# Kernel tuning notes

Measured on AMD Instinct MI355X. Metric: run time of the kernel, lower is better.

The kernel has to match this reference:

```python
import jax, jax.numpy as jnp
import numpy as np


def setup_inputs() -> dict:
    key = jax.random.key(0)
    ks = jax.random.split(key, 8)
    B, S, Nc, C, Cseed = 4, 4096, 8192, 512, 256
    return {
        "query_xyz": jax.random.normal(ks[0], (B, S, 3), dtype=jnp.float32),
        "ref_xyz": jax.random.normal(ks[1], (B, Nc, 3), dtype=jnp.float32),
        "ref_feat": jax.random.normal(ks[2], (B, C, Nc), dtype=jnp.float32),
        "seed_features": jax.random.normal(ks[3], (B, Cseed, S), dtype=jnp.float32),
        "W_seed_proj": jax.random.normal(ks[4], (Cseed, C), dtype=jnp.float32) * 0.02,
        "b_seed_proj": jax.random.normal(ks[5], (Cseed,), dtype=jnp.float32) * 0.02,
        "W_concat_proj": jax.random.normal(ks[6], (Cseed, 2 * Cseed), dtype=jnp.float32) * 0.02,
        "b_concat_proj": jax.random.normal(ks[7], (Cseed,), dtype=jnp.float32) * 0.02,
    }


def _nn_gather(query_xyz, ref_xyz, ref_feat):
    # torch.cdist(p=2) + argmin: argmin over squared distance is identical
    # (sqrt is monotonic), so we skip the sqrt.
    q2 = jnp.sum(query_xyz * query_xyz, axis=-1, keepdims=True)      # (B,S,1)
    r2 = jnp.sum(ref_xyz * ref_xyz, axis=-1)[:, None, :]             # (B,1,Nc)
    qr = jnp.einsum("bsd,bnd->bsn", query_xyz, ref_xyz)              # (B,S,Nc)
    d2 = q2 + r2 - 2.0 * qr                                          # (B,S,Nc)
    idx = jnp.argmin(d2, axis=-1)                                    # (B,S) int
    # gather nearest-neighbor features: (B,C,Nc) -> (B,C,S)
    return jnp.take_along_axis(ref_feat, idx[:, None, :], axis=2)


def reference(query_xyz, ref_xyz, ref_feat, seed_features,
              W_seed_proj, b_seed_proj, W_concat_proj, b_concat_proj):
    lift3d_raw = _nn_gather(query_xyz, ref_xyz, ref_feat)            # (B,C,S)
    # 1x1 Conv1d == channel matmul
    lift3d_seed = jnp.einsum("oc,bcs->bos", W_seed_proj, lift3d_raw) \
                  + b_seed_proj[None, :, None]                       # (B,256,S)
    fused = jnp.concatenate([seed_features, lift3d_seed], axis=1)    # (B,512,S)
    out = jnp.einsum("oc,bcs->bos", W_concat_proj, fused) \
          + b_concat_proj[None, :, None]                             # (B,256,S)
    return out
```

## Files before the change

### kernel.cpp

```cpp
#include <hip/hip_runtime.h>

#define B_   4
#define S_   4096
#define NC   8192
#define C_   512
#define CS   256
#define KTOT 768

typedef __attribute__((ext_vector_type(8))) short short8;
typedef __attribute__((ext_vector_type(4))) float f32x4;

static __device__ __forceinline__ unsigned short f2bf(float x) {
    unsigned u = __builtin_bit_cast(unsigned, x);
    unsigned r = u + 0x7FFFu + ((u >> 16) & 1u);
    return (unsigned short)(r >> 16);
}

__global__ __launch_bounds__(256) void prep_kernel(
        const float* __restrict__ rxyz, float4* __restrict__ refpk,
        const float* __restrict__ Wcat, const float* __restrict__ Wseed,
        unsigned short* __restrict__ Wcomb,
        const float* __restrict__ bseed, const float* __restrict__ bcat,
        float* __restrict__ beff) {
    __shared__ float sa[64][68];
    __shared__ float sbt[64][68];
    int bid = blockIdx.x;
    int tid = threadIdx.x;

    if (bid < 64) {
        int w = tid >> 6, l = tid & 63;
        int o = bid * 4 + w;
        float4 wv = *(const float4*)(Wcat + (size_t)o * 512 + 256 + l * 4);
        float4 bb = *(const float4*)(bseed + l * 4);
        float acc = __fmul_rn(wv.x, bb.x);
        acc = fmaf(wv.y, bb.y, acc);
        acc = fmaf(wv.z, bb.z, acc);
        acc = fmaf(wv.w, bb.w, acc);
        #pragma unroll
        for (int off = 32; off > 0; off >>= 1) acc += __shfl_down(acc, off);
        if (l == 0) beff[o] = acc + bcat[o];
    } else if (bid < 96) {
        int xb = bid - 64;
        int tc = (xb & 7) * 64;
        int to = (xb >> 3) * 64;
        int tx = tid & 15, ty = tid >> 4;
        float acc[4][4] = {};
        for (int kt = 0; kt < 256; kt += 64) {
            __syncthreads();
            #pragma unroll
            for (int r = 0; r < 4; ++r) {
                int oo = r * 16 + ty;
                float4 v = *(const float4*)(Wcat + (size_t)(to + oo) * 512 + 256 + kt + tx * 4);
                sa[oo][tx * 4 + 0] = v.x;
                sa[oo][tx * 4 + 1] = v.y;
                sa[oo][tx * 4 + 2] = v.z;
                sa[oo][tx * 4 + 3] = v.w;
                float4 u = *(const float4*)(Wseed + (size_t)(kt + oo) * 512 + tc + tx * 4);
                sbt[oo][tx * 4 + 0] = u.x;
                sbt[oo][tx * 4 + 1] = u.y;
                sbt[oo][tx * 4 + 2] = u.z;
                sbt[oo][tx * 4 + 3] = u.w;
            }
            __syncthreads();
            for (int k = 0; k < 64; ++k) {
                float a[4], bb2[4];
                #pragma unroll
                for (int i = 0; i < 4; ++i) a[i] = sa[ty * 4 + i][k];
                #pragma unroll
                for (int j = 0; j < 4; ++j) bb2[j] = sbt[k][tx * 4 + j];
                #pragma unroll
                for (int i = 0; i < 4; ++i)
                    #pragma unroll
                    for (int j = 0; j < 4; ++j)
                        acc[i][j] = fmaf(a[i], bb2[j], acc[i][j]);
            }
        }
        #pragma unroll
        for (int i = 0; i < 4; ++i)
            #pragma unroll
            for (int j = 0; j < 4; ++j)
                Wcomb[(size_t)(to + ty * 4 + i) * KTOT + 256 + tc + tx * 4 + j] = f2bf(acc[i][j]);
    } else if (bid < 160) {
        int g = ((bid - 96) * 256 + tid) * 4;
        int o = g >> 8, cc = g & 255;
        float4 v = *(const float4*)(Wcat + (size_t)o * 512 + cc);
        ushort4 ov;
        ov.x = f2bf(v.x); ov.y = f2bf(v.y); ov.z = f2bf(v.z); ov.w = f2bf(v.w);
        *(ushort4*)(Wcomb + (size_t)o * KTOT + cc) = ov;
    } else {
        int gid = (bid - 160) * 256 + tid;
        float x = rxyz[gid * 3 + 0];
        float y = rxyz[gid * 3 + 1];
        float z = rxyz[gid * 3 + 2];
        float r2 = __fadd_rn(__fadd_rn(__fmul_rn(x, x), __fmul_rn(y, y)), __fmul_rn(z, z));
        refpk[gid] = make_float4(x, y, z, r2);
    }
}

__global__ __launch_bounds__(256) void mid_kernel(
        const float* __restrict__ qxyz, const float4* __restrict__ refpk,
        float* __restrict__ pval, int* __restrict__ pidx,
        const float* __restrict__ rf, unsigned short* __restrict__ refT) {
    __shared__ float t[64][65];
    int bid = blockIdx.x;
    int tid = threadIdx.x;

    if (bid % 3 != 0) {
        int id = bid - bid / 3 - 1;
        int b = id >> 10;
        int c0 = ((id >> 7) & 7) * 64;
        int n0 = (id & 127) * 64;
        int tx = tid & 15, ty = tid >> 4;
        #pragma unroll
        for (int r = 0; r < 4; ++r) {
            int cc = r * 16 + ty;
            float4 v = *(const float4*)(rf + ((size_t)b * C_ + c0 + cc) * NC + n0 + tx * 4);
            t[tx * 4 + 0][cc] = v.x;
            t[tx * 4 + 1][cc] = v.y;
            t[tx * 4 + 2][cc] = v.z;
            t[tx * 4 + 3][cc] = v.w;
        }
        __syncthreads();
        #pragma unroll
        for (int r = 0; r < 4; ++r) {
            int n = r * 16 + ty;
            ushort4 o;
            o.x = f2bf(t[n][tx * 4 + 0]);
            o.y = f2bf(t[n][tx * 4 + 1]);
            o.z = f2bf(t[n][tx * 4 + 2]);
            o.w = f2bf(t[n][tx * 4 + 3]);
            *(ushort4*)(refT + ((size_t)b * NC + n0 + n) * C_ + c0 + tx * 4) = o;
        }
    } else {
        int aid = bid / 3;
        int sblk = aid & 127;
        int c = (aid >> 7) & 3;
        int b = aid >> 9;
        int lane = tid & 63;
        int qg = tid >> 6;
        int sbase = sblk * 32 + qg * 8;

        float qx[8], qy[8], qz[8], q2[8];
        #pragma unroll
        for (int q = 0; q < 8; ++q) {
            const float* qp = qxyz + ((size_t)(b * S_ + sbase + q)) * 3;
            qx[q] = qp[0]; qy[q] = qp[1]; qz[q] = qp[2];
            q2[q] = __fadd_rn(__fadd_rn(__fmul_rn(qx[q], qx[q]), __fmul_rn(qy[q], qy[q])),
                              __fmul_rn(qz[q], qz[q]));
        }

        const float4* ep = refpk + (size_t)b * NC + c * 2048 + lane;
        float best[8];
        int bj[8];
        #pragma unroll
        for (int q = 0; q < 8; ++q) { best[q] = 3.4028235e38f; bj[q] = 0; }

        #pragma unroll 4
        for (int j = 0; j < 32; ++j) {
            float4 r = ep[j * 64];
            #pragma unroll
            for (int q = 0; q < 8; ++q) {
                float qr = __fadd_rn(__fadd_rn(__fmul_rn(qx[q], r.x), __fmul_rn(qy[q], r.y)),
                                     __fmul_rn(qz[q], r.z));
                float s = __fadd_rn(q2[q], r.w);
                float d2 = fmaf(qr, -2.0f, s);
                if (d2 < best[q]) { best[q] = d2; bj[q] = j; }
            }
        }

        int bx[8];
        #pragma unroll
        for (int q = 0; q < 8; ++q) bx[q] = c * 2048 + bj[q] * 64 + lane;

        #pragma unroll
        for (int m = 1; m < 64; m <<= 1) {
            #pragma unroll
            for (int q = 0; q < 8; ++q) {
                float vv = __shfl_xor(best[q], m, 64);
                int xx = __shfl_xor(bx[q], m, 64);
                if (vv < best[q] || (vv == best[q] && xx < bx[q])) {
                    best[q] = vv; bx[q] = xx;
                }
            }
        }
        if (lane == 0) {
            #pragma unroll
            for (int q = 0; q < 8; ++q) {
                int qs = b * S_ + sbase + q;
                pval[qs * 4 + c] = best[q];
                pidx[qs * 4 + c] = bx[q];
            }
        }
    }
}

__global__ __launch_bounds__(256) void fused_gemm_kernel(
        const unsigned short* __restrict__ Wcomb,
        const float* __restrict__ seed,
        const unsigned short* __restrict__ refT,
        const float* __restrict__ pval,
        const int* __restrict__ pidx,
        const float* __restrict__ beff,
        float* __restrict__ out) {
    __shared__ __align__(16) unsigned short sA[128][72];
    __shared__ __align__(16) unsigned short sB[32][72];
    __shared__ int sIdx[32];
    __shared__ float sBias[128];

    int tid = threadIdx.x;
    int b = blockIdx.z;
    int m0 = blockIdx.y * 128;
    int s0 = blockIdx.x * 32;
    if (tid < 32) {
        int qs = b * S_ + s0 + tid;
        float v = pval[qs * 4 + 0];
        int x = pidx[qs * 4 + 0];
        #pragma unroll
        for (int c = 1; c < 4; ++c) {
            float vv = pval[qs * 4 + c];
            int xx = pidx[qs * 4 + c];
            if (vv < v || (vv == v && xx < x)) { v = vv; x = xx; }
        }
        sIdx[tid] = x & (NC - 1);
    }
    if (tid < 128) sBias[tid] = beff[m0 + tid];

    int lane = tid & 63;
    int w = tid >> 6;
    int ln = lane & 15;
    int quad = lane >> 4;
    int q8 = quad * 8;

    f32x4 acc[2][2];
    #pragma unroll
    for (int i = 0; i < 2; ++i)
        #pragma unroll
        for (int j = 0; j < 2; ++j)
            acc[i][j] = (f32x4){0.f, 0.f, 0.f, 0.f};

    for (int ks = 0; ks < 12; ++ks) {
        int k0 = ks * 64;
        __syncthreads();
        #pragma unroll
        for (int i = 0; i < 4; ++i) {
            int ch = tid + 256 * i;
            int mm = ch >> 3;
            int kk8 = (ch & 7) << 3;
            *(short8*)&sA[mm][kk8] =
                *(const short8*)(Wcomb + (size_t)(m0 + mm) * KTOT + k0 + kk8);
        }
        if (k0 < 256) {
            int n = tid & 31;
            int kk8 = (tid >> 5) << 3;
            const float* sp = seed + ((size_t)b * CS + k0 + kk8) * S_ + s0 + n;
            unsigned short tmp[8];
            #pragma unroll
            for (int r = 0; r < 8; ++r)
                tmp[r] = f2bf(sp[(size_t)r * S_]);
            *(short8*)&sB[n][kk8] = *(const short8*)tmp;
        } else {
            int n = tid >> 3;
            int kk8 = (tid & 7) << 3;
            const unsigned short* gp =
                refT + ((size_t)b * NC + sIdx[n]) * C_ + (k0 - 256) + kk8;
            *(short8*)&sB[n][kk8] = *(const short8*)gp;
        }
        __syncthreads();
        #pragma unroll
        for (int kf = 0; kf < 2; ++kf) {
            short8 af[2], bfr[2];
            #pragma unroll
            for (int i = 0; i < 2; ++i)
                af[i] = *(const short8*)&sA[w * 32 + i * 16 + ln][kf * 32 + q8];
            #pragma unroll
            for (int j = 0; j < 2; ++j)
                bfr[j] = *(const short8*)&sB[j * 16 + ln][kf * 32 + q8];
            #pragma unroll
            for (int i = 0; i < 2; ++i)
                #pragma unroll
                for (int j = 0; j < 2; ++j)
                    acc[i][j] = __builtin_amdgcn_mfma_f32_16x16x32_bf16(af[i], bfr[j], acc[i][j], 0, 0, 0);
        }
    }

    #pragma unroll
    for (int i = 0; i < 2; ++i) {
        int mb = w * 32 + i * 16 + quad * 4;
        #pragma unroll
        for (int j = 0; j < 2; ++j) {
            int col = s0 + j * 16 + ln;
            #pragma unroll
            for (int r = 0; r < 4; ++r) {
                int m = mb + r;
                out[((size_t)b * CS + m0 + m) * S_ + col] = acc[i][j][r] + sBias[m];
            }
        }
    }
}

extern "C" void kernel_launch(void* const* d_in, const int* in_sizes, int n_in,
                              void* d_out, int out_size, void* d_ws, size_t ws_size,
                              hipStream_t stream) {
    const float* qxyz  = (const float*)d_in[0];
    const float* rxyz  = (const float*)d_in[1];
    const float* rfeat = (const float*)d_in[2];
    const float* seed  = (const float*)d_in[3];
    const float* Wseed = (const float*)d_in[4];
    const float* bseed = (const float*)d_in[5];
    const float* Wcat  = (const float*)d_in[6];
    const float* bcat  = (const float*)d_in[7];
    float* out = (float*)d_out;

    char* ws = (char*)d_ws;
    float* pval           = (float*)(ws);
    int* pidx             = (int*)(ws + 262144);
    float* beff           = (float*)(ws + 524288);
    float4* refpk         = (float4*)(ws + 528384);
    unsigned short* Wcomb = (unsigned short*)(ws + 1052672);
    unsigned short* refT  = (unsigned short*)(ws + 1445888);

    hipLaunchKernelGGL(prep_kernel, dim3(288), dim3(256), 0, stream,
                       rxyz, refpk, Wcat, Wseed, Wcomb, bseed, bcat, beff);
    hipLaunchKernelGGL(mid_kernel, dim3(6144), dim3(256), 0, stream,
                       qxyz, refpk, pval, pidx, rfeat, refT);
    hipLaunchKernelGGL(fused_gemm_kernel, dim3(128, 2, 4), dim3(256), 0, stream,
                       Wcomb, seed, refT, pval, pidx, beff, out);
}
```

Measured before the change: 188.4 us.

## Double-buffer GEMM shared tiles and rebalance NN search into smaller blocks

The fused GEMM now holds two shared-memory buffers and prefetches the next K-slice into registers while MFMAs run on the current one, which removes one barrier per iteration and hides global load latency. The NN-search part of mid_kernel now gives each block 16 queries instead of 32 and interleaves search and transpose blocks 1:1 over a larger grid. It also adds an occupancy hint to the launch bounds. The cost is doubled LDS use and more registers in the GEMM, and more search blocks that each reload the reference points.

```diff
diff --git a/kernel.cpp b/kernel.cpp
--- a/kernel.cpp
+++ b/kernel.cpp
@@ -97,7 +97,7 @@
     }
 }
 
-__global__ __launch_bounds__(256) void mid_kernel(
+__global__ __launch_bounds__(256, 8) void mid_kernel(
         const float* __restrict__ qxyz, const float4* __restrict__ refpk,
         float* __restrict__ pval, int* __restrict__ pidx,
         const float* __restrict__ rf, unsigned short* __restrict__ refT) {
@@ -105,8 +105,8 @@
     int bid = blockIdx.x;
     int tid = threadIdx.x;
 
-    if (bid % 3 != 0) {
-        int id = bid - bid / 3 - 1;
+    if (bid & 1) {
+        int id = bid >> 1;
         int b = id >> 10;
         int c0 = ((id >> 7) & 7) * 64;
         int n0 = (id & 127) * 64;
@@ -132,17 +132,17 @@
             *(ushort4*)(refT + ((size_t)b * NC + n0 + n) * C_ + c0 + tx * 4) = o;
         }
     } else {
-        int aid = bid / 3;
-        int sblk = aid & 127;
-        int c = (aid >> 7) & 3;
-        int b = aid >> 9;
+        int aid = bid >> 1;
+        int sblk = aid & 255;
+        int c = (aid >> 8) & 3;
+        int b = aid >> 10;
         int lane = tid & 63;
         int qg = tid >> 6;
-        int sbase = sblk * 32 + qg * 8;
-
-        float qx[8], qy[8], qz[8], q2[8];
-        #pragma unroll
-        for (int q = 0; q < 8; ++q) {
+        int sbase = sblk * 16 + qg * 4;
+
+        float qx[4], qy[4], qz[4], q2[4];
+        #pragma unroll
+        for (int q = 0; q < 4; ++q) {
             const float* qp = qxyz + ((size_t)(b * S_ + sbase + q)) * 3;
             qx[q] = qp[0]; qy[q] = qp[1]; qz[q] = qp[2];
             q2[q] = __fadd_rn(__fadd_rn(__fmul_rn(qx[q], qx[q]), __fmul_rn(qy[q], qy[q])),
@@ -150,16 +150,16 @@
         }
 
         const float4* ep = refpk + (size_t)b * NC + c * 2048 + lane;
-        float best[8];
-        int bj[8];
-        #pragma unroll
-        for (int q = 0; q < 8; ++q) { best[q] = 3.4028235e38f; bj[q] = 0; }
+        float best[4];
+        int bj[4];
+        #pragma unroll
+        for (int q = 0; q < 4; ++q) { best[q] = 3.4028235e38f; bj[q] = 0; }
 
         #pragma unroll 4
         for (int j = 0; j < 32; ++j) {
             float4 r = ep[j * 64];
             #pragma unroll
-            for (int q = 0; q < 8; ++q) {
+            for (int q = 0; q < 4; ++q) {
                 float qr = __fadd_rn(__fadd_rn(__fmul_rn(qx[q], r.x), __fmul_rn(qy[q], r.y)),
                                      __fmul_rn(qz[q], r.z));
                 float s = __fadd_rn(q2[q], r.w);
@@ -168,14 +168,14 @@
             }
         }
 
-        int bx[8];
-        #pragma unroll
-        for (int q = 0; q < 8; ++q) bx[q] = c * 2048 + bj[q] * 64 + lane;
+        int bx[4];
+        #pragma unroll
+        for (int q = 0; q < 4; ++q) bx[q] = c * 2048 + bj[q] * 64 + lane;
 
         #pragma unroll
         for (int m = 1; m < 64; m <<= 1) {
             #pragma unroll
-            for (int q = 0; q < 8; ++q) {
+            for (int q = 0; q < 4; ++q) {
                 float vv = __shfl_xor(best[q], m, 64);
                 int xx = __shfl_xor(bx[q], m, 64);
                 if (vv < best[q] || (vv == best[q] && xx < bx[q])) {
@@ -185,7 +185,7 @@
         }
         if (lane == 0) {
             #pragma unroll
-            for (int q = 0; q < 8; ++q) {
+            for (int q = 0; q < 4; ++q) {
                 int qs = b * S_ + sbase + q;
                 pval[qs * 4 + c] = best[q];
                 pidx[qs * 4 + c] = bx[q];
@@ -202,8 +202,8 @@
         const int* __restrict__ pidx,
         const float* __restrict__ beff,
         float* __restrict__ out) {
-    __shared__ __align__(16) unsigned short sA[128][72];
-    __shared__ __align__(16) unsigned short sB[32][72];
+    __shared__ __align__(16) unsigned short sA[2][128][72];
+    __shared__ __align__(16) unsigned short sB[2][32][72];
     __shared__ int sIdx[32];
     __shared__ float sBias[128];
 
@@ -231,6 +231,13 @@
     int quad = lane >> 4;
     int q8 = quad * 8;
 
+    int mmb  = tid >> 3;
+    int kk8a = (tid & 7) << 3;
+    const unsigned short* Arow = Wcomb + (size_t)(m0 + mmb) * KTOT + kk8a;
+    int n_s  = tid & 31;
+    int kk8s = (tid >> 5) << 3;
+    int n_g  = tid >> 3;
+
     f32x4 acc[2][2];
     #pragma unroll
     for (int i = 0; i < 2; ++i)
@@ -238,50 +245,70 @@
         for (int j = 0; j < 2; ++j)
             acc[i][j] = (f32x4){0.f, 0.f, 0.f, 0.f};
 
+    short8 ra[4];
+    short8 rb;
+    float rbf[8];
+
+    #define SLOAD(PK) do {                                                         \
+        int pk0 = (PK) * 64;                                                       \
+        _Pragma("unroll")                                                          \
+        for (int i = 0; i < 4; ++i)                                                \
+            ra[i] = *(const short8*)(Arow + (size_t)i * 32 * KTOT + pk0);          \
+        if (pk0 < 256) {                                                           \
+            const float* sp = seed + ((size_t)b * CS + pk0 + kk8s) * S_ + s0 + n_s;\
+            _Pragma("unroll")                                                      \
+            for (int r = 0; r < 8; ++r) rbf[r] = sp[(size_t)r * S_];               \
+        } else {                                                                   \
+            rb = *(const short8*)(refT + ((size_t)b * NC + sIdx[n_g]) * C_         \
+                                  + (pk0 - 256) + kk8a);                           \
+        }                                                                          \
+    } while (0)
+
+    #define SWRITE(BUF, PK) do {                                                   \
+        int pk0 = (PK) * 64;                                                       \
+        _Pragma("unroll")                                                          \
+        for (int i = 0; i < 4; ++i)                                                \
+            *(short8*)&sA[BUF][mmb + 32 * i][kk8a] = ra[i];                        \
+        if (pk0 < 256) {                                                           \
+            unsigned short tmp[8];                                                 \
+            _Pragma("unroll")                                                      \
+            for (int r = 0; r < 8; ++r) tmp[r] = f2bf(rbf[r]);                     \
+            *(short8*)&sB[BUF][n_s][kk8s] = *(const short8*)tmp;                   \
+        } else {                                                                   \
+            *(short8*)&sB[BUF][n_g][kk8a] = rb;                                    \
+        }                                                                          \
+    } while (0)
+
+    SLOAD(0);
+    SWRITE(0, 0);
+    __syncthreads();
+
+    int cur = 0;
     for (int ks = 0; ks < 12; ++ks) {
-        int k0 = ks * 64;
-        __syncthreads();
-        #pragma unroll
-        for (int i = 0; i < 4; ++i) {
-            int ch = tid + 256 * i;
-            int mm = ch >> 3;
-            int kk8 = (ch & 7) << 3;
-            *(short8*)&sA[mm][kk8] =
-                *(const short8*)(Wcomb + (size_t)(m0 + mm) * KTOT + k0 + kk8);
-        }
-        if (k0 < 256) {
-            int n = tid & 31;
-            int kk8 = (tid >> 5) << 3;
-            const float* sp = seed + ((size_t)b * CS + k0 + kk8) * S_ + s0 + n;
-            unsigned short tmp[8];
-            #pragma unroll
-            for (int r = 0; r < 8; ++r)
-                tmp[r] = f2bf(sp[(size_t)r * S_]);
-            *(short8*)&sB[n][kk8] = *(const short8*)tmp;
-        } else {
-            int n = tid >> 3;
-            int kk8 = (tid & 7) << 3;
-            const unsigned short* gp =
-                refT + ((size_t)b * NC + sIdx[n]) * C_ + (k0 - 256) + kk8;
-            *(short8*)&sB[n][kk8] = *(const short8*)gp;
-        }
-        __syncthreads();
+        if (ks < 11) SLOAD(ks + 1);
         #pragma unroll
         for (int kf = 0; kf < 2; ++kf) {
             short8 af[2], bfr[2];
             #pragma unroll
             for (int i = 0; i < 2; ++i)
-                af[i] = *(const short8*)&sA[w * 32 + i * 16 + ln][kf * 32 + q8];
+                af[i] = *(const short8*)&sA[cur][w * 32 + i * 16 + ln][kf * 32 + q8];
             #pragma unroll
             for (int j = 0; j < 2; ++j)
-                bfr[j] = *(const short8*)&sB[j * 16 + ln][kf * 32 + q8];
+                bfr[j] = *(const short8*)&sB[cur][j * 16 + ln][kf * 32 + q8];
             #pragma unroll
             for (int i = 0; i < 2; ++i)
                 #pragma unroll
                 for (int j = 0; j < 2; ++j)
                     acc[i][j] = __builtin_amdgcn_mfma_f32_16x16x32_bf16(af[i], bfr[j], acc[i][j], 0, 0, 0);
         }
-    }
+        if (ks < 11) {
+            SWRITE(cur ^ 1, ks + 1);
+            __syncthreads();
+            cur ^= 1;
+        }
+    }
+    #undef SLOAD
+    #undef SWRITE
 
     #pragma unroll
     for (int i = 0; i < 2; ++i) {
@@ -321,7 +348,7 @@
 
     hipLaunchKernelGGL(prep_kernel, dim3(288), dim3(256), 0, stream,
                        rxyz, refpk, Wcat, Wseed, Wcomb, bseed, bcat, beff);
-    hipLaunchKernelGGL(mid_kernel, dim3(6144), dim3(256), 0, stream,
+    hipLaunchKernelGGL(mid_kernel, dim3(8192), dim3(256), 0, stream,
                        qxyz, refpk, pval, pidx, rfeat, refT);
     hipLaunchKernelGGL(fused_gemm_kernel, dim3(128, 2, 4), dim3(256), 0, stream,
                        Wcomb, seed, refT, pval, pidx, beff, out);
```

Result: slower. 212.8 us (+12.9%).
